# Optimization experiments

Hardware: AMD Instinct MI355X
Metric: run time of the kernel (lower is better)

## Reference

```python
import jax, jax.numpy as jnp
import numpy as np

N, D, E_LOCAL, E_GLOBAL = 50000, 128, 500000, 600000


def gcn_conv(x, W, b, src, dst, w, n):
    """PyG GCNConv with add_self_loops=True, symmetric normalization.

    deg[i] = sum of incoming edge weights at i + 1 (self-loop weight 1)
    norm_e = deg^-1/2[src] * w_e * deg^-1/2[dst]
    out[i] = sum_e norm_e * (xW)[src_e]  +  deg^-1[i] * (xW)[i]  + b
    """
    xw = x @ W  # [n, out]
    deg = jax.ops.segment_sum(w, dst, num_segments=n) + 1.0
    dinv = jnp.where(deg > 0, jax.lax.rsqrt(deg), 0.0)
    norm = dinv[src] * w * dinv[dst]  # [E]
    agg = jax.ops.segment_sum(norm[:, None] * xw[src], dst, num_segments=n)
    self_loop = (dinv * dinv)[:, None] * xw
    return agg + self_loop + b


def setup_inputs() -> dict:
    key = jax.random.key(0)
    ks = jax.random.split(key, 10)
    activity = jax.random.normal(ks[0], (N, D), dtype=jnp.float32)
    learning = jax.random.normal(ks[1], (N, D), dtype=jnp.float32)
    edge_index = jax.random.randint(ks[2], (2, E_LOCAL), 0, N, dtype=jnp.int32)
    edge_weight = jax.random.uniform(ks[3], (E_LOCAL,), dtype=jnp.float32)
    global_edge_index = jax.random.randint(ks[4], (2, E_GLOBAL), 0, N, dtype=jnp.int32)
    global_edge_weight = jax.random.uniform(ks[5], (E_GLOBAL,), dtype=jnp.float32)
    s = 1.0 / np.sqrt(D)
    W_local = jax.random.uniform(ks[6], (D, D), jnp.float32, -s, s)
    b_local = jnp.zeros((D,), jnp.float32)
    W_global = jax.random.uniform(ks[7], (D, D), jnp.float32, -s, s)
    b_global = jnp.zeros((D,), jnp.float32)
    return {
        "activity": activity, "learning": learning,
        "edge_index": edge_index, "edge_weight": edge_weight,
        "global_edge_index": global_edge_index, "global_edge_weight": global_edge_weight,
        "W_local": W_local, "b_local": b_local,
        "W_global": W_global, "b_global": b_global,
    }


def reference(activity, learning, edge_index, edge_weight,
              global_edge_index, global_edge_weight,
              W_local, b_local, W_global, b_global):
    n = activity.shape[0]
    xa = activity + learning
    # Note: GCNConv1 branches in the original are dead code (outputs overwritten);
    # only GCNConv2 (local and global) affect the output.
    xl = gcn_conv(xa, W_local, b_local, edge_index[0], edge_index[1], edge_weight, n)
    xg = gcn_conv(xa, W_global, b_global, global_edge_index[0], global_edge_index[1], global_edge_weight, n)
    wei = jax.nn.sigmoid(xl + xg)
    return 2.0 * activity * wei + 2.0 * learning * (1.0 - wei)
```

## Files before the change

### kernel.cpp

```cpp
#include <hip/hip_runtime.h>

#define DFEAT 128

typedef __attribute__((ext_vector_type(8))) short short8;
typedef __attribute__((ext_vector_type(4))) float float4v;

__device__ __forceinline__ float bf2f(unsigned int h) {
    union { unsigned int u; float f; } v; v.u = h << 16; return v.f;
}
__device__ __forceinline__ unsigned short f2bf(float f) {
    union { float f; unsigned int u; } v; v.f = f;
    unsigned int u = v.u;
    unsigned int lsb = (u >> 16) & 1u;
    u += 0x7fffu + lsb;
    return (unsigned short)(u >> 16);
}
__device__ __forceinline__ float blo(unsigned int u) {
    union { unsigned int x; float f; } v; v.x = u << 16; return v.f;
}
__device__ __forceinline__ float bhi(unsigned int u) {
    union { unsigned int x; float f; } v; v.x = u & 0xffff0000u; return v.f;
}

__global__ __launch_bounds__(256) void zprep_kernel(
    const float* __restrict__ Wl, const float* __restrict__ Wg,
    unsigned short* __restrict__ WT,
    unsigned long long* __restrict__ dc, int n2)
{
    if (blockIdx.x < 128) {
        int idx = blockIdx.x * 256 + threadIdx.x;
        int m = idx >> 14, rem = idx & 16383;
        int k = rem >> 7, c = rem & 127;
        const float* W = m ? Wg : Wl;
        WT[m * 16384 + c * 128 + k] = f2bf(W[k * 128 + c]);
        return;
    }
    int i = (blockIdx.x - 128) * 256 + threadIdx.x;
    if (i < n2) dc[i] = 0ULL;
}

__global__ __launch_bounds__(256) void gemm_hist_kernel(
    const float* __restrict__ A, const float* __restrict__ L,
    const unsigned short* __restrict__ WT,
    unsigned short* __restrict__ xwl, unsigned short* __restrict__ xwg,
    const int* __restrict__ dstL, const float* __restrict__ wL,
    const int* __restrict__ dstG, const float* __restrict__ wG,
    unsigned long long* __restrict__ dc, unsigned short* __restrict__ lp16,
    int El, int Eg, int n, int GB)
{
    if (blockIdx.x >= GB) {
        int e = (blockIdx.x - GB) * 256 + threadIdx.x;
        if (e < El) {
            int t = dstL[e];
            unsigned long long add = (1ULL << 48) | (unsigned long long)(wL[e] * 0x1p40f);
            unsigned long long old = atomicAdd(&dc[t], add);
            lp16[e] = (unsigned short)(old >> 48);
        } else if (e < El + Eg) {
            int e2 = e - El;
            int t = dstG[e2];
            unsigned long long add = (1ULL << 48) | (unsigned long long)(wG[e2] * 0x1p40f);
            unsigned long long old = atomicAdd(&dc[n + t], add);
            lp16[e] = (unsigned short)(old >> 48);
        }
        return;
    }
    const int tid  = threadIdx.x;
    const int wid  = tid >> 6;
    const int lane = tid & 63;
    const int quad = lane >> 4;
    const int cl   = lane & 15;

    int rowa = blockIdx.x * 64 + wid * 16 + cl;
    if (rowa > n - 1) rowa = n - 1;

    const float* Ar = A + (size_t)rowa * DFEAT;
    const float* Lr = L + (size_t)rowa * DFEAT;

    short8 a[4];
    #pragma unroll
    for (int kk = 0; kk < 4; ++kk) {
        const int kb = kk * 32 + quad * 8;
        float4 a0 = *(const float4*)&Ar[kb];
        float4 a1 = *(const float4*)&Ar[kb + 4];
        float4 l0 = *(const float4*)&Lr[kb];
        float4 l1 = *(const float4*)&Lr[kb + 4];
        union { short8 v; unsigned short u[8]; } s;
        s.u[0] = f2bf(a0.x + l0.x); s.u[1] = f2bf(a0.y + l0.y);
        s.u[2] = f2bf(a0.z + l0.z); s.u[3] = f2bf(a0.w + l0.w);
        s.u[4] = f2bf(a1.x + l1.x); s.u[5] = f2bf(a1.y + l1.y);
        s.u[6] = f2bf(a1.z + l1.z); s.u[7] = f2bf(a1.w + l1.w);
        a[kk] = s.v;
    }

    const int rbase = blockIdx.x * 64 + wid * 16 + quad * 4;
    const char* wtb = (const char*)WT + quad * 16;

    #pragma unroll
    for (int m = 0; m < 2; ++m) {
        unsigned short* out = m ? xwg : xwl;
        #pragma unroll
        for (int t = 0; t < 8; ++t) {
            const int col = t * 16 + cl;
            const char* bp = wtb + m * 32768 + col * 256;
            float4v acc = {0.f, 0.f, 0.f, 0.f};
            #pragma unroll
            for (int kk = 0; kk < 4; ++kk) {
                short8 b = *(const short8*)(bp + kk * 64);
                acc = __builtin_amdgcn_mfma_f32_16x16x32_bf16(a[kk], b, acc, 0, 0, 0);
            }
            #pragma unroll
            for (int r = 0; r < 4; ++r) {
                int ro = rbase + r;
                if (ro < n) out[(size_t)ro * DFEAT + col] = f2bf(acc[r]);
            }
        }
    }
}

__global__ __launch_bounds__(256) void scan1_kernel(const unsigned long long* __restrict__ dc,
                                                    int* __restrict__ ptr,
                                                    int* __restrict__ bsum,
                                                    float* __restrict__ dinv, int n)
{
    __shared__ int tmp[256];
    int i = blockIdx.x * 256 + threadIdx.x;
    int v = 0;
    if (i < n) {
        unsigned long long d = dc[i];
        v = (int)(d >> 48);
        dinv[i] = rsqrtf((float)(d & ((1ULL << 48) - 1)) * 0x1p-40f + 1.0f);
    }
    tmp[threadIdx.x] = v;
    __syncthreads();
    for (int off = 1; off < 256; off <<= 1) {
        int t = (threadIdx.x >= off) ? tmp[threadIdx.x - off] : 0;
        __syncthreads();
        tmp[threadIdx.x] += t;
        __syncthreads();
    }
    if (i < n) ptr[i] = tmp[threadIdx.x] - v;
    if (threadIdx.x == 255) bsum[blockIdx.x] = tmp[255];
}

__global__ __launch_bounds__(512) void scan2_kernel(int* __restrict__ bsum, int nb)
{
    __shared__ int tmp[512];
    int i = threadIdx.x;
    int v = (i < nb) ? bsum[i] : 0;
    tmp[i] = v;
    __syncthreads();
    for (int off = 1; off < 512; off <<= 1) {
        int t = (i >= off) ? tmp[i - off] : 0;
        __syncthreads();
        tmp[i] += t;
        __syncthreads();
    }
    if (i < nb) bsum[i] = tmp[i] - v;
}

__global__ __launch_bounds__(256) void edata_write_kernel(
    const int* __restrict__ srcL, const int* __restrict__ dstL, const float* __restrict__ wL,
    const int* __restrict__ srcG, const int* __restrict__ dstG, const float* __restrict__ wG,
    const float* __restrict__ dinv, const int* __restrict__ ptr, const int* __restrict__ bsum,
    const unsigned short* __restrict__ lp16, int2* __restrict__ edata,
    int El, int Eg, int n)
{
    int e = blockIdx.x * 256 + threadIdx.x;
    if (e < El) {
        int s = srcL[e], t = dstL[e];
        float norm = dinv[s] * wL[e] * dinv[t];
        int pos = ptr[t] + bsum[t >> 8] + lp16[e];
        edata[pos] = make_int2(__float_as_int(norm), s);
    } else if (e < El + Eg) {
        int e2 = e - El;
        int s = srcG[e2], t = dstG[e2];
        float norm = dinv[n + s] * wG[e2] * dinv[n + t];
        int tt = n + t;
        int pos = ptr[tt] + bsum[tt >> 8] + lp16[e];
        edata[pos] = make_int2(__float_as_int(norm), s);
    }
}

__global__ __launch_bounds__(256) void gather_kernel(
    const unsigned short* __restrict__ xwl, const unsigned short* __restrict__ xwg,
    const int* __restrict__ ptr, const int* __restrict__ bsum, const int2* __restrict__ edata,
    const float* __restrict__ dinv,
    const float* __restrict__ A, const float* __restrict__ Lr,
    const float* __restrict__ bl, const float* __restrict__ bg,
    float* __restrict__ out, int n, int E)
{
    const int lane = threadIdx.x & 63;
    const int grp  = lane >> 4;
    const int fl   = lane & 15;
    const int node = blockIdx.x * 4 + (threadIdx.x >> 6);
    if (node >= n) return;

    const int i0l = ptr[node] + bsum[node >> 8];
    const int i1l = ptr[node + 1] + bsum[(node + 1) >> 8];
    const int i0g = ptr[n + node] + bsum[(n + node) >> 8];
    const int i1g = (node == n - 1) ? E : ptr[n + node + 1] + bsum[(n + node + 1) >> 8];
    float dl = dinv[node];     dl *= dl;
    float dg = dinv[n + node]; dg *= dg;

    const int fo = fl * 8;
    const size_t nbase = (size_t)node * DFEAT + fo;
    const uint4 svl = *(const uint4*)&xwl[nbase];
    const uint4 svg = *(const uint4*)&xwg[nbase];

    float acc[8] = {0.f, 0.f, 0.f, 0.f, 0.f, 0.f, 0.f, 0.f};

    for (int b0 = i0l; b0 < i1l; b0 += 64) {
        int idx = b0 + lane;
        int2 ed = edata[idx < i1l ? idx : (i1l - 1)];
        float nmv = __int_as_float(ed.x);
        int   sv  = ed.y;
        int cnt = i1l - b0; if (cnt > 64) cnt = 64;
        int iters = (cnt + 3) >> 2;
        #pragma unroll 2
        for (int jj = 0; jj < iters; ++jj) {
            int sl = 4 * jj + grp;
            float nm = __shfl(nmv, sl);
            int   s  = __shfl(sv,  sl);
            if (sl >= cnt) nm = 0.f;
            uint4 pk = *(const uint4*)&xwl[(size_t)s * DFEAT + fo];
            acc[0] += nm * blo(pk.x); acc[1] += nm * bhi(pk.x);
            acc[2] += nm * blo(pk.y); acc[3] += nm * bhi(pk.y);
            acc[4] += nm * blo(pk.z); acc[5] += nm * bhi(pk.z);
            acc[6] += nm * blo(pk.w); acc[7] += nm * bhi(pk.w);
        }
    }
    for (int b0 = i0g; b0 < i1g; b0 += 64) {
        int idx = b0 + lane;
        int2 ed = edata[idx < i1g ? idx : (i1g - 1)];
        float nmv = __int_as_float(ed.x);
        int   sv  = ed.y;
        int cnt = i1g - b0; if (cnt > 64) cnt = 64;
        int iters = (cnt + 3) >> 2;
        #pragma unroll 2
        for (int jj = 0; jj < iters; ++jj) {
            int sl = 4 * jj + grp;
            float nm = __shfl(nmv, sl);
            int   s  = __shfl(sv,  sl);
            if (sl >= cnt) nm = 0.f;
            uint4 pk = *(const uint4*)&xwg[(size_t)s * DFEAT + fo];
            acc[0] += nm * blo(pk.x); acc[1] += nm * bhi(pk.x);
            acc[2] += nm * blo(pk.y); acc[3] += nm * bhi(pk.y);
            acc[4] += nm * blo(pk.z); acc[5] += nm * bhi(pk.z);
            acc[6] += nm * blo(pk.w); acc[7] += nm * bhi(pk.w);
        }
    }

    #pragma unroll
    for (int j = 0; j < 8; ++j) {
        acc[j] += __shfl_xor(acc[j], 16);
        acc[j] += __shfl_xor(acc[j], 32);
    }

    acc[0] += dl * blo(svl.x) + dg * blo(svg.x);
    acc[1] += dl * bhi(svl.x) + dg * bhi(svg.x);
    acc[2] += dl * blo(svl.y) + dg * blo(svg.y);
    acc[3] += dl * bhi(svl.y) + dg * bhi(svg.y);
    acc[4] += dl * blo(svl.z) + dg * blo(svg.z);
    acc[5] += dl * bhi(svl.z) + dg * bhi(svg.z);
    acc[6] += dl * blo(svl.w) + dg * blo(svg.w);
    acc[7] += dl * bhi(svl.w) + dg * bhi(svg.w);

    float s0a = (grp & 1) ? acc[2] : acc[0];
    float s1a = (grp & 1) ? acc[3] : acc[1];
    float s0b = (grp & 1) ? acc[6] : acc[4];
    float s1b = (grp & 1) ? acc[7] : acc[5];
    float v0 = (grp & 2) ? s0b : s0a;
    float v1 = (grp & 2) ? s1b : s1a;

    const int f0 = fo + grp * 2;
    const size_t obase = (size_t)node * DFEAT + f0;
    float2 b1 = *(const float2*)&bl[f0];
    float2 b2 = *(const float2*)&bg[f0];
    float2 a2 = *(const float2*)&A[obase];
    float2 l2 = *(const float2*)&Lr[obase];
    v0 += b1.x + b2.x;
    v1 += b1.y + b2.y;
    float w0 = 1.0f / (1.0f + __expf(-v0));
    float w1 = 1.0f / (1.0f + __expf(-v1));
    float o0 = 2.0f * (a2.x * w0 + l2.x * (1.0f - w0));
    float o1 = 2.0f * (a2.y * w1 + l2.y * (1.0f - w1));
    *(float2*)&out[obase] = make_float2(o0, o1);
}

extern "C" void kernel_launch(void* const* d_in, const int* in_sizes, int n_in,
                              void* d_out, int out_size, void* d_ws, size_t ws_size,
                              hipStream_t stream)
{
    const float* activity = (const float*)d_in[0];
    const float* learning = (const float*)d_in[1];
    const int*   ei  = (const int*)d_in[2];
    const float* ew  = (const float*)d_in[3];
    const int*   gei = (const int*)d_in[4];
    const float* gew = (const float*)d_in[5];
    const float* Wl  = (const float*)d_in[6];
    const float* bl  = (const float*)d_in[7];
    const float* Wg  = (const float*)d_in[8];
    const float* bg  = (const float*)d_in[9];

    const int n  = in_sizes[0] / DFEAT;
    const int El = in_sizes[3];
    const int Eg = in_sizes[5];
    const int n2 = 2 * n;
    const int E  = El + Eg;

    char* ws = (char*)d_ws;
    const size_t xwBytes = (size_t)n * DFEAT * 2;
    unsigned short* xwl = (unsigned short*)ws;
    unsigned short* xwg = (unsigned short*)(ws + xwBytes);
    unsigned long long* dc = (unsigned long long*)(ws + 2 * xwBytes);
    float* dinv = (float*)(ws + 2 * xwBytes + (size_t)n2 * 8);
    int*   ptr  = (int*)(ws + 2 * xwBytes + (size_t)n2 * 12);
    int*   bsum = (int*)(ws + 2 * xwBytes + (size_t)n2 * 16);
    unsigned short* WT = (unsigned short*)(ws + 2 * xwBytes + (size_t)n2 * 16 + 2048);
    int2* edata = (int2*)(ws + 2 * xwBytes + (size_t)n2 * 16 + 2048 + 65536);
    unsigned short* lp16 = (unsigned short*)(ws + 2 * xwBytes + (size_t)n2 * 16 + 2048 + 65536
                                             + (size_t)E * 8);

    const int scanBlocks = (n2 + 255) / 256;
    const int GB = (n + 63) / 64;
    const int HB = (E + 255) / 256;

    zprep_kernel<<<dim3(128 + scanBlocks), dim3(256), 0, stream>>>(Wl, Wg, WT, dc, n2);

    gemm_hist_kernel<<<dim3(GB + HB), dim3(256), 0, stream>>>(
        activity, learning, WT, xwl, xwg,
        ei + El, ew, gei + Eg, gew, dc, lp16, El, Eg, n, GB);

    scan1_kernel<<<dim3(scanBlocks), dim3(256), 0, stream>>>(dc, ptr, bsum, dinv, n2);
    scan2_kernel<<<dim3(1), dim3(512), 0, stream>>>(bsum, scanBlocks);

    edata_write_kernel<<<dim3(HB), dim3(256), 0, stream>>>(
        ei, ei + El, ew, gei, gei + Eg, gew, dinv, ptr, bsum, lp16, edata, El, Eg, n);

    gather_kernel<<<dim3((n + 3) / 4), dim3(256), 0, stream>>>(
        xwl, xwg, ptr, bsum, edata, dinv, activity, learning, bl, bg, (float*)d_out, n, E);
}
```

Baseline: 254.6 us.

## Replace two-pass scan with atomic block bases and pad degree counters

Removes the second scan kernel by having each scan block claim its base offset with a global atomicAdd. Per-node start and count are packed into one 32-bit word so consumers need a single load instead of ptr plus bsum. Degree counters are spread out with a configurable stride to reduce atomic contention on shared cache lines. The gather inner loop unroll is raised. The packed 8-bit count limits per-node degree to 255, and node segment order becomes nondeterministic.

Measured after the change: 261.3 us. +2.6%, slower.

```diff
diff --git a/kernel.cpp b/kernel.cpp
--- a/kernel.cpp
+++ b/kernel.cpp
@@ -25,7 +25,7 @@
 __global__ __launch_bounds__(256) void zprep_kernel(
     const float* __restrict__ Wl, const float* __restrict__ Wg,
     unsigned short* __restrict__ WT,
-    unsigned long long* __restrict__ dc, int n2)
+    unsigned long long* __restrict__ dc, int nz)
 {
     if (blockIdx.x < 128) {
         int idx = blockIdx.x * 256 + threadIdx.x;
@@ -36,7 +36,7 @@
         return;
     }
     int i = (blockIdx.x - 128) * 256 + threadIdx.x;
-    if (i < n2) dc[i] = 0ULL;
+    if (i < nz) dc[i] = 0ULL;
 }
 
 __global__ __launch_bounds__(256) void gemm_hist_kernel(
@@ -46,20 +46,20 @@
     const int* __restrict__ dstL, const float* __restrict__ wL,
     const int* __restrict__ dstG, const float* __restrict__ wG,
     unsigned long long* __restrict__ dc, unsigned short* __restrict__ lp16,
-    int El, int Eg, int n, int GB)
+    int El, int Eg, int n, int GB, int ps)
 {
     if (blockIdx.x >= GB) {
         int e = (blockIdx.x - GB) * 256 + threadIdx.x;
         if (e < El) {
             int t = dstL[e];
             unsigned long long add = (1ULL << 48) | (unsigned long long)(wL[e] * 0x1p40f);
-            unsigned long long old = atomicAdd(&dc[t], add);
+            unsigned long long old = atomicAdd(&dc[(size_t)t << ps], add);
             lp16[e] = (unsigned short)(old >> 48);
         } else if (e < El + Eg) {
             int e2 = e - El;
             int t = dstG[e2];
             unsigned long long add = (1ULL << 48) | (unsigned long long)(wG[e2] * 0x1p40f);
-            unsigned long long old = atomicAdd(&dc[n + t], add);
+            unsigned long long old = atomicAdd(&dc[(size_t)(n + t) << ps], add);
             lp16[e] = (unsigned short)(old >> 48);
         }
         return;
@@ -118,15 +118,17 @@
 }
 
 __global__ __launch_bounds__(256) void scan1_kernel(const unsigned long long* __restrict__ dc,
-                                                    int* __restrict__ ptr,
-                                                    int* __restrict__ bsum,
-                                                    float* __restrict__ dinv, int n)
+                                                    unsigned int* __restrict__ ptrpk,
+                                                    float* __restrict__ dinv,
+                                                    int* __restrict__ gcount,
+                                                    int n2, int ps)
 {
     __shared__ int tmp[256];
+    __shared__ int sbase;
     int i = blockIdx.x * 256 + threadIdx.x;
     int v = 0;
-    if (i < n) {
-        unsigned long long d = dc[i];
+    if (i < n2) {
+        unsigned long long d = dc[(size_t)i << ps];
         v = (int)(d >> 48);
         dinv[i] = rsqrtf((float)(d & ((1ULL << 48) - 1)) * 0x1p-40f + 1.0f);
     }
@@ -138,30 +140,16 @@
         tmp[threadIdx.x] += t;
         __syncthreads();
     }
-    if (i < n) ptr[i] = tmp[threadIdx.x] - v;
-    if (threadIdx.x == 255) bsum[blockIdx.x] = tmp[255];
-}
-
-__global__ __launch_bounds__(512) void scan2_kernel(int* __restrict__ bsum, int nb)
-{
-    __shared__ int tmp[512];
-    int i = threadIdx.x;
-    int v = (i < nb) ? bsum[i] : 0;
-    tmp[i] = v;
+    if (threadIdx.x == 255) sbase = atomicAdd(gcount, tmp[255]);
     __syncthreads();
-    for (int off = 1; off < 512; off <<= 1) {
-        int t = (i >= off) ? tmp[i - off] : 0;
-        __syncthreads();
-        tmp[i] += t;
-        __syncthreads();
-    }
-    if (i < nb) bsum[i] = tmp[i] - v;
+    if (i < n2)
+        ptrpk[i] = (unsigned int)(sbase + tmp[threadIdx.x] - v) | ((unsigned int)v << 24);
 }
 
 __global__ __launch_bounds__(256) void edata_write_kernel(
     const int* __restrict__ srcL, const int* __restrict__ dstL, const float* __restrict__ wL,
     const int* __restrict__ srcG, const int* __restrict__ dstG, const float* __restrict__ wG,
-    const float* __restrict__ dinv, const int* __restrict__ ptr, const int* __restrict__ bsum,
+    const float* __restrict__ dinv, const unsigned int* __restrict__ ptrpk,
     const unsigned short* __restrict__ lp16, int2* __restrict__ edata,
     int El, int Eg, int n)
 {
@@ -169,25 +157,24 @@
     if (e < El) {
         int s = srcL[e], t = dstL[e];
         float norm = dinv[s] * wL[e] * dinv[t];
-        int pos = ptr[t] + bsum[t >> 8] + lp16[e];
+        int pos = (int)(ptrpk[t] & 0xFFFFFFu) + lp16[e];
         edata[pos] = make_int2(__float_as_int(norm), s);
     } else if (e < El + Eg) {
         int e2 = e - El;
         int s = srcG[e2], t = dstG[e2];
         float norm = dinv[n + s] * wG[e2] * dinv[n + t];
-        int tt = n + t;
-        int pos = ptr[tt] + bsum[tt >> 8] + lp16[e];
+        int pos = (int)(ptrpk[n + t] & 0xFFFFFFu) + lp16[e];
         edata[pos] = make_int2(__float_as_int(norm), s);
     }
 }
 
 __global__ __launch_bounds__(256) void gather_kernel(
     const unsigned short* __restrict__ xwl, const unsigned short* __restrict__ xwg,
-    const int* __restrict__ ptr, const int* __restrict__ bsum, const int2* __restrict__ edata,
+    const unsigned int* __restrict__ ptrpk, const int2* __restrict__ edata,
     const float* __restrict__ dinv,
     const float* __restrict__ A, const float* __restrict__ Lr,
     const float* __restrict__ bl, const float* __restrict__ bg,
-    float* __restrict__ out, int n, int E)
+    float* __restrict__ out, int n)
 {
     const int lane = threadIdx.x & 63;
     const int grp  = lane >> 4;
@@ -195,10 +182,12 @@
     const int node = blockIdx.x * 4 + (threadIdx.x >> 6);
     if (node >= n) return;
 
-    const int i0l = ptr[node] + bsum[node >> 8];
-    const int i1l = ptr[node + 1] + bsum[(node + 1) >> 8];
-    const int i0g = ptr[n + node] + bsum[(n + node) >> 8];
-    const int i1g = (node == n - 1) ? E : ptr[n + node + 1] + bsum[(n + node + 1) >> 8];
+    const unsigned int pl = ptrpk[node];
+    const unsigned int pg = ptrpk[n + node];
+    const int i0l = (int)(pl & 0xFFFFFFu);
+    const int i1l = i0l + (int)(pl >> 24);
+    const int i0g = (int)(pg & 0xFFFFFFu);
+    const int i1g = i0g + (int)(pg >> 24);
     float dl = dinv[node];     dl *= dl;
     float dg = dinv[n + node]; dg *= dg;
 
@@ -216,7 +205,7 @@
         int   sv  = ed.y;
         int cnt = i1l - b0; if (cnt > 64) cnt = 64;
         int iters = (cnt + 3) >> 2;
-        #pragma unroll 2
+        #pragma unroll 4
         for (int jj = 0; jj < iters; ++jj) {
             int sl = 4 * jj + grp;
             float nm = __shfl(nmv, sl);
@@ -236,7 +225,7 @@
         int   sv  = ed.y;
         int cnt = i1g - b0; if (cnt > 64) cnt = 64;
         int iters = (cnt + 3) >> 2;
-        #pragma unroll 2
+        #pragma unroll 4
         for (int jj = 0; jj < iters; ++jj) {
             int sl = 4 * jj + grp;
             float nm = __shfl(nmv, sl);
@@ -310,33 +299,45 @@
 
     char* ws = (char*)d_ws;
     const size_t xwBytes = (size_t)n * DFEAT * 2;
-    unsigned short* xwl = (unsigned short*)ws;
-    unsigned short* xwg = (unsigned short*)(ws + xwBytes);
-    unsigned long long* dc = (unsigned long long*)(ws + 2 * xwBytes);
-    float* dinv = (float*)(ws + 2 * xwBytes + (size_t)n2 * 8);
-    int*   ptr  = (int*)(ws + 2 * xwBytes + (size_t)n2 * 12);
-    int*   bsum = (int*)(ws + 2 * xwBytes + (size_t)n2 * 16);
-    unsigned short* WT = (unsigned short*)(ws + 2 * xwBytes + (size_t)n2 * 16 + 2048);
-    int2* edata = (int2*)(ws + 2 * xwBytes + (size_t)n2 * 16 + 2048 + 65536);
-    unsigned short* lp16 = (unsigned short*)(ws + 2 * xwBytes + (size_t)n2 * 16 + 2048 + 65536
+    const size_t fixedBytes = 2 * xwBytes
+                            + (size_t)n2 * 4
+                            + (size_t)n2 * 4
+                            + 65536
+                            + (size_t)E * 8
+                            + (size_t)E * 2;
+
+    int ps = 3;
+    while (ps > 0 &&
+           fixedBytes + (((size_t)n2 << ps) + 16) * 8 > ws_size) --ps;
+
+    unsigned short* xwl  = (unsigned short*)ws;
+    unsigned short* xwg  = (unsigned short*)(ws + xwBytes);
+    float*          dinv = (float*)(ws + 2 * xwBytes);
+    unsigned int*   ptrpk= (unsigned int*)(ws + 2 * xwBytes + (size_t)n2 * 4);
+    unsigned short* WT   = (unsigned short*)(ws + 2 * xwBytes + (size_t)n2 * 8);
+    int2*           edata= (int2*)(ws + 2 * xwBytes + (size_t)n2 * 8 + 65536);
+    unsigned short* lp16 = (unsigned short*)(ws + 2 * xwBytes + (size_t)n2 * 8 + 65536
                                              + (size_t)E * 8);
-
-    const int scanBlocks = (n2 + 255) / 256;
+    unsigned long long* dc = (unsigned long long*)(ws + fixedBytes);
+    int* gcount = (int*)(dc + ((size_t)n2 << ps));
+
+    const int nz = (int)(((size_t)n2 << ps) + 8);
+    const int zb = (nz + 255) / 256;
     const int GB = (n + 63) / 64;
     const int HB = (E + 255) / 256;
-
-    zprep_kernel<<<dim3(128 + scanBlocks), dim3(256), 0, stream>>>(Wl, Wg, WT, dc, n2);
+    const int scanBlocks = (n2 + 255) / 256;
+
+    zprep_kernel<<<dim3(128 + zb), dim3(256), 0, stream>>>(Wl, Wg, WT, dc, nz);
 
     gemm_hist_kernel<<<dim3(GB + HB), dim3(256), 0, stream>>>(
         activity, learning, WT, xwl, xwg,
-        ei + El, ew, gei + Eg, gew, dc, lp16, El, Eg, n, GB);
-
-    scan1_kernel<<<dim3(scanBlocks), dim3(256), 0, stream>>>(dc, ptr, bsum, dinv, n2);
-    scan2_kernel<<<dim3(1), dim3(512), 0, stream>>>(bsum, scanBlocks);
+        ei + El, ew, gei + Eg, gew, dc, lp16, El, Eg, n, GB, ps);
+
+    scan1_kernel<<<dim3(scanBlocks), dim3(256), 0, stream>>>(dc, ptrpk, dinv, gcount, n2, ps);
 
     edata_write_kernel<<<dim3(HB), dim3(256), 0, stream>>>(
-        ei, ei + El, ew, gei, gei + Eg, gew, dinv, ptr, bsum, lp16, edata, El, Eg, n);
+        ei, ei + El, ew, gei, gei + Eg, gew, dinv, ptrpk, lp16, edata, El, Eg, n);
 
     gather_kernel<<<dim3((n + 3) / 4), dim3(256), 0, stream>>>(
-        xwl, xwg, ptr, bsum, edata, dinv, activity, learning, bl, bg, (float*)d_out, n, E);
-}
+        xwl, xwg, ptrpk, edata, dinv, activity, learning, bl, bg, (float*)d_out, n);
+}
```
